# Performance work log

Measured on AMD Instinct MI355X. Metric: run time of the kernel, lower is better.

The kernel has to match this reference:

```python
import jax, jax.numpy as jnp
import numpy as np

N = 500          # number of brain regions (nodes)
T = 20000        # Euler integration steps
DT = 0.05        # integration step size
SQDT = float(np.sqrt(DT))
NOISE_STD = 0.02 # state-noise amplitude


def setup_inputs() -> dict:
    key = jax.random.key(0)
    ks = jax.random.split(key, 7)
    sc = jax.random.uniform(ks[0], (N, N), dtype=jnp.float32)
    sc = 0.5 * (sc + sc.T)
    sc = sc / jnp.sum(sc, axis=1, keepdims=True)  # row-normalized SC (deg_i = 1)
    x0 = 0.1 * jax.random.normal(ks[1], (N,), dtype=jnp.float32)
    y0 = 0.1 * jax.random.normal(ks[2], (N,), dtype=jnp.float32)
    a = jax.random.uniform(ks[3], (N,), dtype=jnp.float32)           # bifurcation param per node, in [0,1)
    omega = 0.1 + 0.4 * jax.random.uniform(ks[4], (N,), dtype=jnp.float32)  # intrinsic angular frequency
    noise = NOISE_STD * jax.random.normal(ks[5], (T, N, 2), dtype=jnp.float32)
    g = 0.05 * jnp.ones((1,), dtype=jnp.float32)                     # global coupling
    return {"sc": sc, "x0": x0, "y0": y0, "a": a, "omega": omega, "noise": noise, "g": g}


def reference(sc, x0, y0, a, omega, noise, g):
    """Coupled Hopf oscillators, Euler-Maruyama over T steps.
    Returns the x-trajectory [T, N]."""
    deg = jnp.sum(sc, axis=1)  # [N], in-strength for diffusive coupling

    def step(carry, nz):
        x, y = carry                       # [N], [N]
        r2 = x * x + y * y                 # |z|^2
        cx = sc @ x - deg * x              # diffusive coupling sum_j SC_ij (x_j - x_i)
        cy = sc @ y - deg * y
        dx = (a - r2) * x - omega * y + g * cx
        dy = (a - r2) * y + omega * x + g * cy
        xn = x + DT * dx + SQDT * nz[:, 0]
        yn = y + DT * dy + SQDT * nz[:, 1]
        return (xn, yn), xn

    _, xs = jax.lax.scan(step, (x0, y0), noise)
    return xs  # [T, N]
```

## Files before the change

### kernel.cpp

```cpp
#include <hip/hip_runtime.h>

#define NN    500
#define TT    20000
#define NPAD  512
#define NBLK  8
#define NROW  64
#define TPB   512
#define RPT   4
#define CPT   16
#define SLOTW 4
#define DTC   0.05f
#define SQDTC 0.22360679774997896f

typedef unsigned int u32x4 __attribute__((ext_vector_type(4)));

__device__ __forceinline__ void store_coh_u128(u32x4* p, u32x4 v) {
    asm volatile("global_store_dwordx4 %0, %1, off sc0 sc1" :: "v"(p), "v"(v) : "memory");
}
__device__ __forceinline__ u32x4 load_coh_u128(const u32x4* p) {
    u32x4 v;
    asm volatile("global_load_dwordx4 %0, %1, off sc0 sc1\n\t"
                 "s_waitcnt vmcnt(0)" : "=v"(v) : "v"(p) : "memory");
    return v;
}

__global__ __launch_bounds__(1024) void hopf_init_ws(u32x4* pub) {
    int i = blockIdx.x * blockDim.x + threadIdx.x;
    if (i < 2 * NPAD * SLOTW) pub[i] = (u32x4){0u, 0u, 0u, 0u};
}

__global__ __launch_bounds__(TPB) void hopf_main(
    const float* __restrict__ sc, const float* __restrict__ x0,
    const float* __restrict__ y0, const float* __restrict__ aa,
    const float* __restrict__ om, const float* __restrict__ noise,
    const float* __restrict__ gg, float* __restrict__ out,
    u32x4* __restrict__ pub)
{
    const int tid  = threadIdx.x;
    const int blk  = blockIdx.x;
    const int cgrp = tid & 31;
    const int rgrp = tid >> 5;
    const int r0   = blk * NROW + rgrp * RPT;

    __shared__ __align__(16) float2 xy[NPAD];
    __shared__ __align__(16) float2 own[NROW];

    float scr[RPT][CPT];
#pragma unroll
    for (int r = 0; r < RPT; ++r) {
        int row = r0 + r;
#pragma unroll
        for (int c = 0; c < CPT; ++c) {
            int col = cgrp + 32 * c;
            scr[r][c] = (row < NN && col < NN) ? sc[row * NN + col] : 0.0f;
        }
    }

    float dsum[RPT];
#pragma unroll
    for (int r = 0; r < RPT; ++r) {
        float s = 0.f;
#pragma unroll
        for (int c = 0; c < CPT; ++c) s += scr[r][c];
        dsum[r] = s;
    }
#pragma unroll
    for (int m = 16; m >= 1; m >>= 1) {
#pragma unroll
        for (int r = 0; r < RPT; ++r) dsum[r] += __shfl_xor(dsum[r], m, 32);
    }

#pragma unroll
    for (int r = 0; r < RPT; ++r)
#pragma unroll
        for (int c = 0; c < CPT; ++c)
            asm volatile("" : "+v"(scr[r][c]));

    float a_i = 0.f, om_i = 0.f, deg_i = 0.f;
    int myrow = -1;
    if (cgrp < RPT) {
        int row = r0 + cgrp;
        deg_i = (cgrp == 0) ? dsum[0] : (cgrp == 1) ? dsum[1]
              : (cgrp == 2) ? dsum[2] : dsum[3];
        if (row < NN) { myrow = row; a_i = aa[row]; om_i = om[row]; }
    }
    const float g = gg[0];
    const int obase = blk * NROW;

    xy[tid] = (tid < NN) ? make_float2(x0[tid], y0[tid]) : make_float2(0.f, 0.f);
    __syncthreads();

    float2 nz = make_float2(0.f, 0.f);
    if (myrow >= 0) nz = *(const float2*)(noise + 2 * (size_t)myrow);

    for (int t = 0; t < TT; ++t) {
        const int p = t & 1;
        float2 nz_next = make_float2(0.f, 0.f);
        if (myrow >= 0 && t + 1 < TT)
            nz_next = *(const float2*)(noise + (size_t)(t + 1) * (2 * NN) + 2 * (size_t)myrow);

        float2 acc[RPT];
#pragma unroll
        for (int r = 0; r < RPT; ++r) acc[r] = make_float2(0.f, 0.f);
#pragma unroll
        for (int c = 0; c < CPT; ++c) {
            float2 w = xy[cgrp + 32 * c];
#pragma unroll
            for (int r = 0; r < RPT; ++r) {
                acc[r].x += scr[r][c] * w.x;
                acc[r].y += scr[r][c] * w.y;
            }
        }
#pragma unroll
        for (int m = 16; m >= 1; m >>= 1) {
#pragma unroll
            for (int r = 0; r < RPT; ++r) {
                acc[r].x += __shfl_xor(acc[r].x, m, 32);
                acc[r].y += __shfl_xor(acc[r].y, m, 32);
            }
        }

        if (myrow >= 0) {
            float sx = (cgrp == 0) ? acc[0].x : (cgrp == 1) ? acc[1].x
                     : (cgrp == 2) ? acc[2].x : acc[3].x;
            float sy = (cgrp == 0) ? acc[0].y : (cgrp == 1) ? acc[1].y
                     : (cgrp == 2) ? acc[2].y : acc[3].y;
            float2 cur = xy[myrow];
            float r2 = cur.x * cur.x + cur.y * cur.y;
            float cx = sx - deg_i * cur.x;
            float cy = sy - deg_i * cur.y;
            float dx = (a_i - r2) * cur.x - om_i * cur.y + g * cx;
            float dy = (a_i - r2) * cur.y + om_i * cur.x + g * cy;
            float xn = cur.x + DTC * dx + SQDTC * nz.x;
            float yn = cur.y + DTC * dy + SQDTC * nz.y;
            out[(size_t)t * NN + myrow] = xn;
            u32x4 pkt = { __float_as_uint(xn), (unsigned)(t + 1),
                          __float_as_uint(yn), (unsigned)(t + 1) };
            store_coh_u128(&pub[((size_t)p * NPAD + myrow) * SLOTW], pkt);
            own[myrow - obase] = make_float2(xn, yn);
        }
        nz = nz_next;

        if (t == TT - 1) break;

        __syncthreads();

        if (tid < NN) {
            if (tid >= obase && tid < obase + NROW) {
                xy[tid] = own[tid - obase];
            } else {
                const u32x4* slot = &pub[((size_t)p * NPAD + tid) * SLOTW];
                u32x4 v;
                do {
                    v = load_coh_u128(slot);
                } while ((int)v.y < t + 1 || (int)v.w < t + 1);
                xy[tid] = make_float2(__uint_as_float(v.x), __uint_as_float(v.z));
            }
        }
        __syncthreads();
    }
}

extern "C" void kernel_launch(void* const* d_in, const int* in_sizes, int n_in,
                              void* d_out, int out_size, void* d_ws, size_t ws_size,
                              hipStream_t stream) {
    const float* sc = (const float*)d_in[0];
    const float* x0 = (const float*)d_in[1];
    const float* y0 = (const float*)d_in[2];
    const float* aa = (const float*)d_in[3];
    const float* om = (const float*)d_in[4];
    const float* nz = (const float*)d_in[5];
    const float* gg = (const float*)d_in[6];
    float* out = (float*)d_out;

    u32x4* pub = (u32x4*)d_ws;

    hipLaunchKernelGGL(hopf_init_ws, dim3(4), dim3(1024), 0, stream, pub);
    hipLaunchKernelGGL(hopf_main, dim3(NBLK), dim3(TPB), 0, stream,
                       sc, x0, y0, aa, om, nz, gg, out, pub);
}
```

Baseline: 43.02 ms.

## Batch noise loads and output stores across 8 steps, compact publish slots

Restructures the time loop into blocks of 8 steps. Noise for all 8 steps is prefetched with inline-asm async loads and waited on once, and the x outputs are buffered in registers and written after each block. The publish slots also shrink from 64-byte to 16-byte stride, packing them more densely. The aim is to take global load and store latency off the per-step critical path of the cross-block spin-wait. In exchange it uses more registers, and the denser slots may share cache lines and cause extra coherence traffic.

Measured after the change: 43.75 ms. About the same (+1.7%).

```diff
diff --git a/kernel.cpp b/kernel.cpp
--- a/kernel.cpp
+++ b/kernel.cpp
@@ -8,11 +8,12 @@
 #define TPB   512
 #define RPT   4
 #define CPT   16
-#define SLOTW 4
+#define KB    8
 #define DTC   0.05f
 #define SQDTC 0.22360679774997896f
 
 typedef unsigned int u32x4 __attribute__((ext_vector_type(4)));
+typedef float        f32x2 __attribute__((ext_vector_type(2)));
 
 __device__ __forceinline__ void store_coh_u128(u32x4* p, u32x4 v) {
     asm volatile("global_store_dwordx4 %0, %1, off sc0 sc1" :: "v"(p), "v"(v) : "memory");
@@ -23,10 +24,13 @@
                  "s_waitcnt vmcnt(0)" : "=v"(v) : "v"(p) : "memory");
     return v;
 }
+__device__ __forceinline__ void load_async_f2(f32x2* dst, const float* p) {
+    asm volatile("global_load_dwordx2 %0, %1, off" : "=v"(*dst) : "v"(p) : "memory");
+}
 
 __global__ __launch_bounds__(1024) void hopf_init_ws(u32x4* pub) {
     int i = blockIdx.x * blockDim.x + threadIdx.x;
-    if (i < 2 * NPAD * SLOTW) pub[i] = (u32x4){0u, 0u, 0u, 0u};
+    if (i < 2 * NPAD) pub[i] = (u32x4){0u, 0u, 0u, 0u};
 }
 
 __global__ __launch_bounds__(TPB) void hopf_main(
@@ -87,77 +91,92 @@
     const float g = gg[0];
     const int obase = blk * NROW;
 
+    const float* nrow = noise + 2 * (size_t)(myrow >= 0 ? myrow : 0);
+
     xy[tid] = (tid < NN) ? make_float2(x0[tid], y0[tid]) : make_float2(0.f, 0.f);
     __syncthreads();
 
-    float2 nz = make_float2(0.f, 0.f);
-    if (myrow >= 0) nz = *(const float2*)(noise + 2 * (size_t)myrow);
-
-    for (int t = 0; t < TT; ++t) {
-        const int p = t & 1;
-        float2 nz_next = make_float2(0.f, 0.f);
-        if (myrow >= 0 && t + 1 < TT)
-            nz_next = *(const float2*)(noise + (size_t)(t + 1) * (2 * NN) + 2 * (size_t)myrow);
-
-        float2 acc[RPT];
-#pragma unroll
-        for (int r = 0; r < RPT; ++r) acc[r] = make_float2(0.f, 0.f);
-#pragma unroll
-        for (int c = 0; c < CPT; ++c) {
-            float2 w = xy[cgrp + 32 * c];
-#pragma unroll
-            for (int r = 0; r < RPT; ++r) {
-                acc[r].x += scr[r][c] * w.x;
-                acc[r].y += scr[r][c] * w.y;
+    for (int tb = 0; tb < TT; tb += KB) {
+        f32x2 nzb[KB];
+#pragma unroll
+        for (int k = 0; k < KB; ++k)
+            load_async_f2(&nzb[k], nrow + (size_t)(tb + k) * (2 * NN));
+
+        float xnb[KB];
+
+#pragma unroll
+        for (int k = 0; k < KB; ++k) {
+            const int t = tb + k;
+            const int p = t & 1;
+
+            float2 acc[RPT];
+#pragma unroll
+            for (int r = 0; r < RPT; ++r) acc[r] = make_float2(0.f, 0.f);
+#pragma unroll
+            for (int c = 0; c < CPT; ++c) {
+                float2 w = xy[cgrp + 32 * c];
+#pragma unroll
+                for (int r = 0; r < RPT; ++r) {
+                    acc[r].x += scr[r][c] * w.x;
+                    acc[r].y += scr[r][c] * w.y;
+                }
+            }
+#pragma unroll
+            for (int m = 16; m >= 1; m >>= 1) {
+#pragma unroll
+                for (int r = 0; r < RPT; ++r) {
+                    acc[r].x += __shfl_xor(acc[r].x, m, 32);
+                    acc[r].y += __shfl_xor(acc[r].y, m, 32);
+                }
+            }
+
+            if (k == 0) asm volatile("s_waitcnt vmcnt(0)" ::: "memory");
+
+            if (myrow >= 0) {
+                float sx = (cgrp == 0) ? acc[0].x : (cgrp == 1) ? acc[1].x
+                         : (cgrp == 2) ? acc[2].x : acc[3].x;
+                float sy = (cgrp == 0) ? acc[0].y : (cgrp == 1) ? acc[1].y
+                         : (cgrp == 2) ? acc[2].y : acc[3].y;
+                float2 cur = xy[myrow];
+                float r2 = cur.x * cur.x + cur.y * cur.y;
+                float cx = sx - deg_i * cur.x;
+                float cy = sy - deg_i * cur.y;
+                float dx = (a_i - r2) * cur.x - om_i * cur.y + g * cx;
+                float dy = (a_i - r2) * cur.y + om_i * cur.x + g * cy;
+                float xn = cur.x + DTC * dx + SQDTC * nzb[k].x;
+                float yn = cur.y + DTC * dy + SQDTC * nzb[k].y;
+                xnb[k] = xn;
+                u32x4 pkt = { __float_as_uint(xn), (unsigned)(t + 1),
+                              __float_as_uint(yn), (unsigned)(t + 1) };
+                store_coh_u128(&pub[(size_t)p * NPAD + myrow], pkt);
+                own[myrow - obase] = make_float2(xn, yn);
+            }
+
+            if (t < TT - 1) {
+                __syncthreads();
+
+                if (tid < NN) {
+                    if (tid >= obase && tid < obase + NROW) {
+                        xy[tid] = own[tid - obase];
+                    } else {
+                        const u32x4* slot = &pub[(size_t)p * NPAD + tid];
+                        u32x4 v;
+                        do {
+                            v = load_coh_u128(slot);
+                        } while ((int)v.y < t + 1 || (int)v.w < t + 1);
+                        xy[tid] = make_float2(__uint_as_float(v.x),
+                                              __uint_as_float(v.z));
+                    }
+                }
+                __syncthreads();
             }
         }
-#pragma unroll
-        for (int m = 16; m >= 1; m >>= 1) {
-#pragma unroll
-            for (int r = 0; r < RPT; ++r) {
-                acc[r].x += __shfl_xor(acc[r].x, m, 32);
-                acc[r].y += __shfl_xor(acc[r].y, m, 32);
-            }
+
+        if (myrow >= 0) {
+#pragma unroll
+            for (int k = 0; k < KB; ++k)
+                out[(size_t)(tb + k) * NN + myrow] = xnb[k];
         }
-
-        if (myrow >= 0) {
-            float sx = (cgrp == 0) ? acc[0].x : (cgrp == 1) ? acc[1].x
-                     : (cgrp == 2) ? acc[2].x : acc[3].x;
-            float sy = (cgrp == 0) ? acc[0].y : (cgrp == 1) ? acc[1].y
-                     : (cgrp == 2) ? acc[2].y : acc[3].y;
-            float2 cur = xy[myrow];
-            float r2 = cur.x * cur.x + cur.y * cur.y;
-            float cx = sx - deg_i * cur.x;
-            float cy = sy - deg_i * cur.y;
-            float dx = (a_i - r2) * cur.x - om_i * cur.y + g * cx;
-            float dy = (a_i - r2) * cur.y + om_i * cur.x + g * cy;
-            float xn = cur.x + DTC * dx + SQDTC * nz.x;
-            float yn = cur.y + DTC * dy + SQDTC * nz.y;
-            out[(size_t)t * NN + myrow] = xn;
-            u32x4 pkt = { __float_as_uint(xn), (unsigned)(t + 1),
-                          __float_as_uint(yn), (unsigned)(t + 1) };
-            store_coh_u128(&pub[((size_t)p * NPAD + myrow) * SLOTW], pkt);
-            own[myrow - obase] = make_float2(xn, yn);
-        }
-        nz = nz_next;
-
-        if (t == TT - 1) break;
-
-        __syncthreads();
-
-        if (tid < NN) {
-            if (tid >= obase && tid < obase + NROW) {
-                xy[tid] = own[tid - obase];
-            } else {
-                const u32x4* slot = &pub[((size_t)p * NPAD + tid) * SLOTW];
-                u32x4 v;
-                do {
-                    v = load_coh_u128(slot);
-                } while ((int)v.y < t + 1 || (int)v.w < t + 1);
-                xy[tid] = make_float2(__uint_as_float(v.x), __uint_as_float(v.z));
-            }
-        }
-        __syncthreads();
     }
 }
 
@@ -175,7 +194,7 @@
 
     u32x4* pub = (u32x4*)d_ws;
 
-    hipLaunchKernelGGL(hopf_init_ws, dim3(4), dim3(1024), 0, stream, pub);
+    hipLaunchKernelGGL(hopf_init_ws, dim3(1), dim3(1024), 0, stream, pub);
     hipLaunchKernelGGL(hopf_main, dim3(NBLK), dim3(TPB), 0, stream,
                        sc, x0, y0, aa, om, nz, gg, out, pub);
 }
```
